# Performance work log

Hardware: AMD Instinct MI355X
Metric: run time of the kernel (lower is better)

## Reference

```python
import jax, jax.numpy as jnp
import numpy as np

EPS = 1e-5

def _ln(x, g, b):
    m = jnp.mean(x, axis=-1, keepdims=True)
    v = jnp.var(x, axis=-1, keepdims=True)
    return (x - m) / jnp.sqrt(v + EPS) * g + b

def setup_inputs() -> dict:
    key = jax.random.key(0)
    ks = jax.random.split(key, 16)
    B, N, CZ, C = 1, 512, 128, 16
    s_cz = 1.0 / np.sqrt(CZ)
    s_c = 1.0 / np.sqrt(C)
    def lin(k, fan_in, shape):
        return jax.random.uniform(k, shape, jnp.float32, -1.0, 1.0) / np.sqrt(fan_in)
    return {
        'x': jax.random.normal(ks[0], (B, N, N, CZ), jnp.float32),
        'Wa1': lin(ks[1], CZ, (CZ, C)), 'ba1': lin(ks[2], CZ, (C,)),
        'Wa2': lin(ks[3], CZ, (CZ, C)), 'ba2': lin(ks[4], CZ, (C,)),
        'Wb1': lin(ks[5], CZ, (CZ, C)), 'bb1': lin(ks[6], CZ, (C,)),
        'Wb2': lin(ks[7], CZ, (CZ, C)), 'bb2': lin(ks[8], CZ, (C,)),
        'ln2_g': jnp.ones((C,), jnp.float32), 'ln2_b': jnp.zeros((C,), jnp.float32),
        'Wg': lin(ks[9], CZ, (CZ, CZ)), 'bg': lin(ks[10], CZ, (CZ,)),
        'Wz': lin(ks[11], C, (C, CZ)), 'bz': lin(ks[12], C, (CZ,)),
    }

def reference(x, Wa1, ba1, Wa2, ba2, Wb1, bb1, Wb2, bb2, ln2_g, ln2_b, Wg, bg, Wz, bz):
    # NOTE: original code computes z=ln1(x) then overwrites z=x, so ln1 is a no-op.
    direction = 'outgoing'
    a = jax.nn.sigmoid((x @ Wa1 + ba1) * (x @ Wa2 + ba2))  # [B,N,N,c]
    b = jax.nn.sigmoid((x @ Wb1 + bb1) * (x @ Wb2 + bb2))  # [B,N,N,c]
    if direction == 'incoming':
        a = jnp.swapaxes(a, 1, 2)
        b = jnp.swapaxes(b, 1, 2)
    g = jax.nn.sigmoid(x @ Wg + bg)  # [B,N,N,c_z]
    # z[b,i,j,c] = sum_k a[b,i,k,c] * b[b,k,j,c]  (per-channel triangle matmul)
    z = jnp.einsum('bikc,bkjc->bijc', a, b)
    return g * (_ln(z, ln2_g, ln2_b) @ Wz + bz)
```

## Files before the change

### kernel.cpp

```cpp
#include <hip/hip_runtime.h>


#define NN 512
#define PP (NN*NN)
#define CZD 128
#define CD 16
#define LN_EPS 1e-5f

typedef unsigned short u16;
typedef __bf16 bf16x8 __attribute__((ext_vector_type(8)));
typedef float  f32x4  __attribute__((ext_vector_type(4)));

#define OFF_A  0u
#define OFF_B  8388608u
#define OFF_Z  16777216u
#define OFF_G  33554432u
#define OFF_WT 100663296u
#define OFF_BC 100712448u

__device__ __forceinline__ float bf2f(u16 u) {
    union { unsigned int i; float f; } v; v.i = ((unsigned int)u) << 16; return v.f;
}
__device__ __forceinline__ u16 f2bf(float f) {
    union { __bf16 b; u16 u; } v; v.b = (__bf16)f; return v.u;
}
__device__ __forceinline__ float sigmoidf(float x) { return 1.0f / (1.0f + __expf(-x)); }

__device__ __forceinline__ int swz(int row, int bytecol) {
    return row * 256 + ((((bytecol >> 4) + row) & 15) << 4) + (bytecol & 15);
}

__global__ void pack_w(const float* __restrict__ Wa1, const float* __restrict__ Wa2,
                       const float* __restrict__ Wb1, const float* __restrict__ Wb2,
                       const float* __restrict__ Wg,
                       const float* __restrict__ ba1, const float* __restrict__ ba2,
                       const float* __restrict__ bb1, const float* __restrict__ bb2,
                       const float* __restrict__ bg,
                       u16* __restrict__ wt, float* __restrict__ bc) {
    int idx = blockIdx.x * 256 + threadIdx.x;
    int n = idx >> 7, k = idx & 127;
    float v;
    if      (n < 16) v = Wa1[k * CD + n];
    else if (n < 32) v = Wa2[k * CD + (n - 16)];
    else if (n < 48) v = Wb1[k * CD + (n - 32)];
    else if (n < 64) v = Wb2[k * CD + (n - 48)];
    else             v = Wg [k * CZD + (n - 64)];
    wt[n * CZD + k] = f2bf(v);
    if (idx < 192) {
        float b;
        if      (idx < 16) b = ba1[idx];
        else if (idx < 32) b = ba2[idx - 16];
        else if (idx < 48) b = bb1[idx - 32];
        else if (idx < 64) b = bb2[idx - 48];
        else               b = bg [idx - 64];
        bc[idx] = b;
    }
}

__global__ __launch_bounds__(512, 4) void proj_kernel(const float* __restrict__ x,
                                                      const u16* __restrict__ wt,
                                                      const float* __restrict__ bc,
                                                      u16* __restrict__ a_ws, u16* __restrict__ b_ws,
                                                      u16* __restrict__ g_ws) {
    __shared__ __align__(16) char lds[49152];
    char* Wl = lds;
    char* aT = lds;
    char* bT = lds + 4096;
    char* gT = lds + 8192;
    const int t = threadIdx.x;
    const int wv = t >> 6, lane = t & 63, l16 = lane & 15, quad = lane >> 4;
    const long pos0 = (long)blockIdx.x * 128;

    const float* xrow = x + (pos0 + wv * 16 + l16) * CZD + quad * 8;
    float4 xa[4][2];
#pragma unroll
    for (int ks = 0; ks < 4; ++ks) {
        xa[ks][0] = *reinterpret_cast<const float4*>(xrow + ks * 32);
        xa[ks][1] = *reinterpret_cast<const float4*>(xrow + ks * 32 + 4);
    }

#pragma unroll
    for (int i = 0; i < 6; ++i) {
        int c = t + 512 * i;
        int n = c >> 4, g = c & 15;
        uint4 v = *reinterpret_cast<const uint4*>(wt + n * CZD + g * 8);
        *reinterpret_cast<uint4*>(Wl + swz(n, g * 16)) = v;
    }

    bf16x8 af[4];
#pragma unroll
    for (int ks = 0; ks < 4; ++ks) {
        union { u16 s[8]; bf16x8 v; } tb;
        tb.s[0] = f2bf(xa[ks][0].x); tb.s[1] = f2bf(xa[ks][0].y);
        tb.s[2] = f2bf(xa[ks][0].z); tb.s[3] = f2bf(xa[ks][0].w);
        tb.s[4] = f2bf(xa[ks][1].x); tb.s[5] = f2bf(xa[ks][1].y);
        tb.s[6] = f2bf(xa[ks][1].z); tb.s[7] = f2bf(xa[ks][1].w);
        af[ks] = tb.v;
    }
    __syncthreads();

    f32x4 acc[12];
#pragma unroll
    for (int ct = 0; ct < 12; ++ct) acc[ct] = (f32x4){0.f, 0.f, 0.f, 0.f};
#pragma unroll
    for (int ks = 0; ks < 4; ++ks)
#pragma unroll
        for (int ct = 0; ct < 12; ++ct) {
            bf16x8 wb = *reinterpret_cast<const bf16x8*>(Wl + swz(ct * 16 + l16, ks * 64 + quad * 16));
            acc[ct] = __builtin_amdgcn_mfma_f32_16x16x32_bf16(af[ks], wb, acc[ct], 0, 0, 0);
        }
    __syncthreads();

    {
        const float ba1 = bc[l16], ba2 = bc[16 + l16], bb1 = bc[32 + l16], bb2 = bc[48 + l16];
        u16 av[4], bv[4];
#pragma unroll
        for (int r = 0; r < 4; ++r) {
            av[r] = f2bf(sigmoidf((acc[0][r] + ba1) * (acc[1][r] + ba2)));
            bv[r] = f2bf(sigmoidf((acc[2][r] + bb1) * (acc[3][r] + bb2)));
        }
        *reinterpret_cast<uint2*>(aT + swz(l16, wv * 32 + quad * 8)) = *reinterpret_cast<const uint2*>(av);
        *reinterpret_cast<uint2*>(bT + swz(l16, wv * 32 + quad * 8)) = *reinterpret_cast<const uint2*>(bv);
#pragma unroll
        for (int ct = 0; ct < 8; ++ct) {
            const float bgv = bc[64 + ct * 16 + l16];
#pragma unroll
            for (int r = 0; r < 4; ++r) {
                int pos = wv * 16 + quad * 4 + r;
                *reinterpret_cast<u16*>(gT + swz(pos, ct * 32 + l16 * 2)) =
                    f2bf(sigmoidf(acc[4 + ct][r] + bgv));
            }
        }
    }
    __syncthreads();

    if (t < 256) {
        int ch = t >> 4, i = t & 15;
        uint4 v = *reinterpret_cast<const uint4*>(aT + swz(ch, i * 16));
        *reinterpret_cast<uint4*>(a_ws + (long)ch * PP + pos0 + i * 8) = v;
    } else {
        int u = t - 256;
        int ch = u >> 4, i = u & 15;
        uint4 v = *reinterpret_cast<const uint4*>(bT + swz(ch, i * 16));
        *reinterpret_cast<uint4*>(b_ws + (long)ch * PP + pos0 + i * 8) = v;
    }
#pragma unroll
    for (int i = 0; i < 4; ++i) {
        int c = t + 512 * i;
        int pos = c >> 4, g = c & 15;
        uint4 v = *reinterpret_cast<const uint4*>(gT + swz(pos, g * 16));
        *reinterpret_cast<uint4*>(g_ws + (pos0 + pos) * CZD + g * 8) = v;
    }
}

__global__ __launch_bounds__(512) void tri_kernel(const u16* __restrict__ a_ws,
                                                  const u16* __restrict__ b_ws,
                                                  float* __restrict__ z_ws) {
    __shared__ __align__(16) char Alds[16384];
    __shared__ __align__(16) char Btl [16384];
    const int t = threadIdx.x;
    const int wv = t >> 6, lane = t & 63, l16 = lane & 15, quad = lane >> 4;
    const int wr = wv >> 2, wc = wv & 3;
    const int c = blockIdx.y;
    const int i0 = (blockIdx.x >> 2) * 128, j0 = (blockIdx.x & 3) * 128;
    const u16* Ap = a_ws + (long)c * PP;
    const u16* Bp = b_ws + (long)c * PP;

    f32x4 acc[4][2];
#pragma unroll
    for (int m = 0; m < 4; ++m)
#pragma unroll
        for (int n = 0; n < 2; ++n) acc[m][n] = (f32x4){0.f, 0.f, 0.f, 0.f};

    for (int k0 = 0; k0 < NN; k0 += 64) {
#pragma unroll
        for (int i = 0; i < 2; ++i) {
            int ch = t + 512 * i;
            int r = ch >> 3, ko = (ch & 7) * 8;
            uint4 v = *reinterpret_cast<const uint4*>(Ap + (long)(i0 + r) * NN + k0 + ko);
            *reinterpret_cast<uint4*>(Alds + r * 128 + ((ko * 2) ^ ((r & 7) << 4))) = v;
        }
#pragma unroll
        for (int i = 0; i < 2; ++i) {
            int chk = t + 512 * i;
            int k = chk >> 4, jo = (chk & 15) * 8;
            union { uint4 v; u16 s[8]; } tb;
            tb.v = *reinterpret_cast<const uint4*>(Bp + (long)(k0 + k) * NN + j0 + jo);
            const int kg = k >> 3, kl = (k & 7) * 2;
#pragma unroll
            for (int jj = 0; jj < 8; ++jj) {
                int j = jo + jj;
                int gran = ((kg ^ (j & 7)) + (j >> 3)) & 7;
                *reinterpret_cast<u16*>(Btl + j * 128 + gran * 16 + kl) = tb.s[jj];
            }
        }
        __syncthreads();
#pragma unroll
        for (int ks = 0; ks < 2; ++ks) {
            bf16x8 af[4];
#pragma unroll
            for (int m = 0; m < 4; ++m) {
                int row = wr * 64 + m * 16 + l16;
                af[m] = *reinterpret_cast<const bf16x8*>(
                    Alds + row * 128 + ((ks * 64 + quad * 16) ^ ((row & 7) << 4)));
            }
#pragma unroll
            for (int n = 0; n < 2; ++n) {
                int jrow = wc * 32 + n * 16 + l16;
                int gran = (((ks * 4 + quad) ^ (jrow & 7)) + (jrow >> 3)) & 7;
                bf16x8 bf = *reinterpret_cast<const bf16x8*>(Btl + jrow * 128 + gran * 16);
#pragma unroll
                for (int m = 0; m < 4; ++m)
                    acc[m][n] = __builtin_amdgcn_mfma_f32_16x16x32_bf16(af[m], bf, acc[m][n], 0, 0, 0);
            }
        }
        __syncthreads();
    }
    float* Zp = z_ws + (long)c * PP;
#pragma unroll
    for (int m = 0; m < 4; ++m)
#pragma unroll
        for (int n = 0; n < 2; ++n)
#pragma unroll
            for (int r = 0; r < 4; ++r)
                Zp[(long)(i0 + wr * 64 + m * 16 + quad * 4 + r) * NN + j0 + wc * 32 + n * 16 + l16]
                    = acc[m][n][r];
}

__global__ __launch_bounds__(512) void out_kernel(const float* __restrict__ z_ws,
                                                  const u16* __restrict__ g_ws,
                                                  const float* __restrict__ Wz, const float* __restrict__ bz,
                                                  const float* __restrict__ lng, const float* __restrict__ lnb,
                                                  float* __restrict__ out) {
    __shared__ __align__(16) float zt[16][128];
    __shared__ __align__(16) float nl[128][20];
    __shared__ __align__(16) float wzs[16][128];
    __shared__ float bzl[128];
    __shared__ float lg[16], lb[16];
    const int t = threadIdx.x;
    const long tbase = (long)blockIdx.x * 256;

    const int zch = t >> 5, zoff = (t & 31) * 4;
    const float* zp = z_ws + (long)zch * PP + tbase + zoff;
    const float4 zv0 = *reinterpret_cast<const float4*>(zp);
    const float4 zv1 = *reinterpret_cast<const float4*>(zp + 128);

    {
        int idx = t * 4;
        const float4 v = *reinterpret_cast<const float4*>(Wz + idx);
        *reinterpret_cast<float4*>(&wzs[idx >> 7][idx & 127]) = v;
    }
    if (t < 128)      bzl[t] = bz[t];
    else if (t < 144) lg[t - 128] = lng[t - 128];
    else if (t < 160) lb[t - 144] = lnb[t - 144];
    *reinterpret_cast<float4*>(&zt[zch][zoff]) = zv0;
    __syncthreads();

    const int czp = (t & 63) * 2, pg = t >> 6;
    float wzr[32];
#pragma unroll
    for (int c0 = 0; c0 < 16; ++c0) {
        wzr[2 * c0]     = wzs[c0][czp];
        wzr[2 * c0 + 1] = wzs[c0][czp + 1];
    }
    const float bz0 = bzl[czp], bz1 = bzl[czp + 1];
    const unsigned int* gp = reinterpret_cast<const unsigned int*>(g_ws);

#pragma unroll
    for (int it = 0; it < 2; ++it) {
        const long pos0 = tbase + it * 128;
        {
            int p = t & 127, cgr = t >> 7;
            float m = 0.f;
#pragma unroll
            for (int c0 = 0; c0 < 16; ++c0) m += zt[c0][p];
            m *= (1.f / 16.f);
            float v = 0.f;
#pragma unroll
            for (int c0 = 0; c0 < 16; ++c0) { float d = zt[c0][p] - m; v += d * d; }
            v *= (1.f / 16.f);
            float s = rsqrtf(v + LN_EPS);
#pragma unroll
            for (int cc = 0; cc < 4; ++cc) {
                int c0 = cgr * 4 + cc;
                nl[p][c0] = (zt[c0][p] - m) * s * lg[c0] + lb[c0];
            }
        }
        __syncthreads();
        if (it == 0)
            *reinterpret_cast<float4*>(&zt[zch][zoff]) = zv1;

#pragma unroll
        for (int pp2 = 0; pp2 < 16; ++pp2) {
            int p = pg * 16 + pp2;
            const float4* np = reinterpret_cast<const float4*>(&nl[p][0]);
            float y0 = bz0, y1 = bz1;
#pragma unroll
            for (int c4 = 0; c4 < 4; ++c4) {
                float4 nv = np[c4];
                y0 += nv.x * wzr[(c4 * 4 + 0) * 2] + nv.y * wzr[(c4 * 4 + 1) * 2] +
                      nv.z * wzr[(c4 * 4 + 2) * 2] + nv.w * wzr[(c4 * 4 + 3) * 2];
                y1 += nv.x * wzr[(c4 * 4 + 0) * 2 + 1] + nv.y * wzr[(c4 * 4 + 1) * 2 + 1] +
                      nv.z * wzr[(c4 * 4 + 2) * 2 + 1] + nv.w * wzr[(c4 * 4 + 3) * 2 + 1];
            }
            long o = (pos0 + p) * CZD + czp;
            unsigned int gg = gp[o >> 1];
            float g0 = bf2f((u16)(gg & 0xffffu));
            float g1 = bf2f((u16)(gg >> 16));
            float2 res; res.x = g0 * y0; res.y = g1 * y1;
            *reinterpret_cast<float2*>(out + o) = res;
        }
        __syncthreads();
    }
}

extern "C" void kernel_launch(void* const* d_in, const int* in_sizes, int n_in,
                              void* d_out, int out_size, void* d_ws, size_t ws_size,
                              hipStream_t stream) {
    const float* x   = (const float*)d_in[0];
    const float* Wa1 = (const float*)d_in[1];
    const float* ba1 = (const float*)d_in[2];
    const float* Wa2 = (const float*)d_in[3];
    const float* ba2 = (const float*)d_in[4];
    const float* Wb1 = (const float*)d_in[5];
    const float* bb1 = (const float*)d_in[6];
    const float* Wb2 = (const float*)d_in[7];
    const float* bb2 = (const float*)d_in[8];
    const float* lng = (const float*)d_in[9];
    const float* lnb = (const float*)d_in[10];
    const float* Wg  = (const float*)d_in[11];
    const float* bg  = (const float*)d_in[12];
    const float* Wz  = (const float*)d_in[13];
    const float* bz  = (const float*)d_in[14];
    float* out = (float*)d_out;
    char* ws = (char*)d_ws;
    u16*   a_ws = (u16*)(ws + OFF_A);
    u16*   b_ws = (u16*)(ws + OFF_B);
    float* z_ws = (float*)(ws + OFF_Z);
    u16*   g_ws = (u16*)(ws + OFF_G);
    u16*   wt   = (u16*)(ws + OFF_WT);
    float* bc   = (float*)(ws + OFF_BC);

    hipLaunchKernelGGL(pack_w, dim3(96), dim3(256), 0, stream,
                       Wa1, Wa2, Wb1, Wb2, Wg, ba1, ba2, bb1, bb2, bg, wt, bc);
    hipLaunchKernelGGL(proj_kernel, dim3(2048), dim3(512), 0, stream, x, wt, bc, a_ws, b_ws, g_ws);
    hipLaunchKernelGGL(tri_kernel, dim3(16, 16), dim3(512), 0, stream, a_ws, b_ws, z_ws);
    hipLaunchKernelGGL(out_kernel, dim3(1024), dim3(512), 0, stream, z_ws, g_ws, Wz, bz, lng, lnb, out);
}
```

Measured before the change: 310.2 us.

## Make projection kernel persistent over 4 tiles with prefetch; pack B transpose stores

Each proj_kernel block now handles 512 positions in four sub-tiles instead of 128. The packed weights are loaded into LDS once per block and reused across all four, and x for the next sub-tile is prefetched while the current MFMAs run. Outputs are written straight to global memory instead of being staged through LDS, which drops two barriers but makes the a/b and g stores narrow and scattered. Separately, the tri_kernel B-tile transpose now loads two k rows per thread and writes packed 32-bit pairs to LDS, halving the number of scattered 16-bit stores.

Result: slower. 318.6 us (+2.7%).

```diff
diff --git a/kernel.cpp b/kernel.cpp
--- a/kernel.cpp
+++ b/kernel.cpp
@@ -62,14 +62,15 @@
                                                       const float* __restrict__ bc,
                                                       u16* __restrict__ a_ws, u16* __restrict__ b_ws,
                                                       u16* __restrict__ g_ws) {
-    __shared__ __align__(16) char lds[49152];
-    char* Wl = lds;
-    char* aT = lds;
-    char* bT = lds + 4096;
-    char* gT = lds + 8192;
+    __shared__ __align__(16) char Wl[49152];
     const int t = threadIdx.x;
     const int wv = t >> 6, lane = t & 63, l16 = lane & 15, quad = lane >> 4;
-    const long pos0 = (long)blockIdx.x * 128;
+    const long pos0 = (long)blockIdx.x * 512;
+
+    const float ba1 = bc[l16], ba2 = bc[16 + l16], bb1 = bc[32 + l16], bb2 = bc[48 + l16];
+    float bgv[8];
+#pragma unroll
+    for (int ct = 0; ct < 8; ++ct) bgv[ct] = bc[64 + ct * 16 + l16];
 
     const float* xrow = x + (pos0 + wv * 16 + l16) * CZD + quad * 8;
     float4 xa[4][2];
@@ -99,57 +100,58 @@
     }
     __syncthreads();
 
-    f32x4 acc[12];
-#pragma unroll
-    for (int ct = 0; ct < 12; ++ct) acc[ct] = (f32x4){0.f, 0.f, 0.f, 0.f};
-#pragma unroll
-    for (int ks = 0; ks < 4; ++ks)
-#pragma unroll
-        for (int ct = 0; ct < 12; ++ct) {
-            bf16x8 wb = *reinterpret_cast<const bf16x8*>(Wl + swz(ct * 16 + l16, ks * 64 + quad * 16));
-            acc[ct] = __builtin_amdgcn_mfma_f32_16x16x32_bf16(af[ks], wb, acc[ct], 0, 0, 0);
-        }
-    __syncthreads();
-
-    {
-        const float ba1 = bc[l16], ba2 = bc[16 + l16], bb1 = bc[32 + l16], bb2 = bc[48 + l16];
-        u16 av[4], bv[4];
-#pragma unroll
-        for (int r = 0; r < 4; ++r) {
-            av[r] = f2bf(sigmoidf((acc[0][r] + ba1) * (acc[1][r] + ba2)));
-            bv[r] = f2bf(sigmoidf((acc[2][r] + bb1) * (acc[3][r] + bb2)));
-        }
-        *reinterpret_cast<uint2*>(aT + swz(l16, wv * 32 + quad * 8)) = *reinterpret_cast<const uint2*>(av);
-        *reinterpret_cast<uint2*>(bT + swz(l16, wv * 32 + quad * 8)) = *reinterpret_cast<const uint2*>(bv);
-#pragma unroll
-        for (int ct = 0; ct < 8; ++ct) {
-            const float bgv = bc[64 + ct * 16 + l16];
+#pragma unroll
+    for (int p = 0; p < 4; ++p) {
+        const long prow = pos0 + p * 128 + wv * 16 + quad * 4;
+
+        f32x4 acc[12];
+#pragma unroll
+        for (int ct = 0; ct < 12; ++ct) acc[ct] = (f32x4){0.f, 0.f, 0.f, 0.f};
+#pragma unroll
+        for (int ks = 0; ks < 4; ++ks)
+#pragma unroll
+            for (int ct = 0; ct < 12; ++ct) {
+                bf16x8 wb = *reinterpret_cast<const bf16x8*>(Wl + swz(ct * 16 + l16, ks * 64 + quad * 16));
+                acc[ct] = __builtin_amdgcn_mfma_f32_16x16x32_bf16(af[ks], wb, acc[ct], 0, 0, 0);
+            }
+
+        if (p < 3) {
+            const float* xr2 = xrow + (p + 1) * 128 * CZD;
+#pragma unroll
+            for (int ks = 0; ks < 4; ++ks) {
+                xa[ks][0] = *reinterpret_cast<const float4*>(xr2 + ks * 32);
+                xa[ks][1] = *reinterpret_cast<const float4*>(xr2 + ks * 32 + 4);
+            }
+        }
+
+        {
+            u16 av[4], bv[4];
 #pragma unroll
             for (int r = 0; r < 4; ++r) {
-                int pos = wv * 16 + quad * 4 + r;
-                *reinterpret_cast<u16*>(gT + swz(pos, ct * 32 + l16 * 2)) =
-                    f2bf(sigmoidf(acc[4 + ct][r] + bgv));
-            }
-        }
-    }
-    __syncthreads();
-
-    if (t < 256) {
-        int ch = t >> 4, i = t & 15;
-        uint4 v = *reinterpret_cast<const uint4*>(aT + swz(ch, i * 16));
-        *reinterpret_cast<uint4*>(a_ws + (long)ch * PP + pos0 + i * 8) = v;
-    } else {
-        int u = t - 256;
-        int ch = u >> 4, i = u & 15;
-        uint4 v = *reinterpret_cast<const uint4*>(bT + swz(ch, i * 16));
-        *reinterpret_cast<uint4*>(b_ws + (long)ch * PP + pos0 + i * 8) = v;
-    }
-#pragma unroll
-    for (int i = 0; i < 4; ++i) {
-        int c = t + 512 * i;
-        int pos = c >> 4, g = c & 15;
-        uint4 v = *reinterpret_cast<const uint4*>(gT + swz(pos, g * 16));
-        *reinterpret_cast<uint4*>(g_ws + (pos0 + pos) * CZD + g * 8) = v;
+                av[r] = f2bf(sigmoidf((acc[0][r] + ba1) * (acc[1][r] + ba2)));
+                bv[r] = f2bf(sigmoidf((acc[2][r] + bb1) * (acc[3][r] + bb2)));
+            }
+            *reinterpret_cast<uint2*>(a_ws + (long)l16 * PP + prow) = *reinterpret_cast<const uint2*>(av);
+            *reinterpret_cast<uint2*>(b_ws + (long)l16 * PP + prow) = *reinterpret_cast<const uint2*>(bv);
+            u16* gbase = g_ws + prow * CZD + l16;
+#pragma unroll
+            for (int ct = 0; ct < 8; ++ct)
+#pragma unroll
+                for (int r = 0; r < 4; ++r)
+                    gbase[r * CZD + ct * 16] = f2bf(sigmoidf(acc[4 + ct][r] + bgv[ct]));
+        }
+
+        if (p < 3) {
+#pragma unroll
+            for (int ks = 0; ks < 4; ++ks) {
+                union { u16 s[8]; bf16x8 v; } tb;
+                tb.s[0] = f2bf(xa[ks][0].x); tb.s[1] = f2bf(xa[ks][0].y);
+                tb.s[2] = f2bf(xa[ks][0].z); tb.s[3] = f2bf(xa[ks][0].w);
+                tb.s[4] = f2bf(xa[ks][1].x); tb.s[5] = f2bf(xa[ks][1].y);
+                tb.s[6] = f2bf(xa[ks][1].z); tb.s[7] = f2bf(xa[ks][1].w);
+                af[ks] = tb.v;
+            }
+        }
     }
 }
 
@@ -180,18 +182,19 @@
             uint4 v = *reinterpret_cast<const uint4*>(Ap + (long)(i0 + r) * NN + k0 + ko);
             *reinterpret_cast<uint4*>(Alds + r * 128 + ((ko * 2) ^ ((r & 7) << 4))) = v;
         }
-#pragma unroll
-        for (int i = 0; i < 2; ++i) {
-            int chk = t + 512 * i;
-            int k = chk >> 4, jo = (chk & 15) * 8;
-            union { uint4 v; u16 s[8]; } tb;
-            tb.v = *reinterpret_cast<const uint4*>(Bp + (long)(k0 + k) * NN + j0 + jo);
+        {
+            int kp = t >> 4, jo = (t & 15) * 8;
+            int k = kp * 2;
+            union { uint4 v; u16 s[8]; } t0, t1;
+            t0.v = *reinterpret_cast<const uint4*>(Bp + (long)(k0 + k) * NN + j0 + jo);
+            t1.v = *reinterpret_cast<const uint4*>(Bp + (long)(k0 + k + 1) * NN + j0 + jo);
             const int kg = k >> 3, kl = (k & 7) * 2;
 #pragma unroll
             for (int jj = 0; jj < 8; ++jj) {
                 int j = jo + jj;
                 int gran = ((kg ^ (j & 7)) + (j >> 3)) & 7;
-                *reinterpret_cast<u16*>(Btl + j * 128 + gran * 16 + kl) = tb.s[jj];
+                unsigned int pk = (unsigned int)t0.s[jj] | ((unsigned int)t1.s[jj] << 16);
+                *reinterpret_cast<unsigned int*>(Btl + j * 128 + gran * 16 + kl) = pk;
             }
         }
         __syncthreads();
@@ -343,7 +346,7 @@
 
     hipLaunchKernelGGL(pack_w, dim3(96), dim3(256), 0, stream,
                        Wa1, Wa2, Wb1, Wb2, Wg, ba1, ba2, bb1, bb2, bg, wt, bc);
-    hipLaunchKernelGGL(proj_kernel, dim3(2048), dim3(512), 0, stream, x, wt, bc, a_ws, b_ws, g_ws);
+    hipLaunchKernelGGL(proj_kernel, dim3(512), dim3(512), 0, stream, x, wt, bc, a_ws, b_ws, g_ws);
     hipLaunchKernelGGL(tri_kernel, dim3(16, 16), dim3(512), 0, stream, a_ws, b_ws, z_ws);
     hipLaunchKernelGGL(out_kernel, dim3(1024), dim3(512), 0, stream, z_ws, g_ws, Wz, bz, lng, lnb, out);
 }
```

## Prefetch next K-tile into registers and pack B transpose stores as 32-bit

Applied to the files above, without the earlier changes.

The triangle-matmul kernel now issues the global loads for the next 64-wide K tile right after the barrier, so they overlap with the MFMA work on the current tile, instead of loading and then storing synchronously at the top of each iteration. The B tile thread mapping changes so each thread loads two adjacent k rows and writes packed 32-bit pairs into the transposed LDS layout, which halves the number of scalar LDS stores. This costs extra registers for the prefetch buffers, which may affect occupancy at 512 threads per block.

After: 308.5 us (median of 2 runs). Within noise of the previous version (-0.5%).

```diff
diff --git a/kernel.cpp b/kernel.cpp
--- a/kernel.cpp
+++ b/kernel.cpp
@@ -166,35 +166,46 @@
     const u16* Ap = a_ws + (long)c * PP;
     const u16* Bp = b_ws + (long)c * PP;
 
+    const int ar0 = t >> 3,          ako0 = (t & 7) * 8;
+    const int ar1 = (t + 512) >> 3,  ako1 = ((t + 512) & 7) * 8;
+    const int bk  = (t >> 4) * 2,    bjo  = (t & 15) * 8;
+    const int bkg = bk >> 3,         bkl  = (bk & 7) * 2;
+
     f32x4 acc[4][2];
 #pragma unroll
     for (int m = 0; m < 4; ++m)
 #pragma unroll
         for (int n = 0; n < 2; ++n) acc[m][n] = (f32x4){0.f, 0.f, 0.f, 0.f};
 
-    for (int k0 = 0; k0 < NN; k0 += 64) {
-#pragma unroll
-        for (int i = 0; i < 2; ++i) {
-            int ch = t + 512 * i;
-            int r = ch >> 3, ko = (ch & 7) * 8;
-            uint4 v = *reinterpret_cast<const uint4*>(Ap + (long)(i0 + r) * NN + k0 + ko);
-            *reinterpret_cast<uint4*>(Alds + r * 128 + ((ko * 2) ^ ((r & 7) << 4))) = v;
-        }
-#pragma unroll
-        for (int i = 0; i < 2; ++i) {
-            int chk = t + 512 * i;
-            int k = chk >> 4, jo = (chk & 15) * 8;
-            union { uint4 v; u16 s[8]; } tb;
-            tb.v = *reinterpret_cast<const uint4*>(Bp + (long)(k0 + k) * NN + j0 + jo);
-            const int kg = k >> 3, kl = (k & 7) * 2;
+    uint4 aR0 = *reinterpret_cast<const uint4*>(Ap + (long)(i0 + ar0) * NN + ako0);
+    uint4 aR1 = *reinterpret_cast<const uint4*>(Ap + (long)(i0 + ar1) * NN + ako1);
+    uint4 bR0 = *reinterpret_cast<const uint4*>(Bp + (long)(bk)     * NN + j0 + bjo);
+    uint4 bR1 = *reinterpret_cast<const uint4*>(Bp + (long)(bk + 1) * NN + j0 + bjo);
+
+    for (int s = 0; s < 8; ++s) {
+        *reinterpret_cast<uint4*>(Alds + ar0 * 128 + ((ako0 * 2) ^ ((ar0 & 7) << 4))) = aR0;
+        *reinterpret_cast<uint4*>(Alds + ar1 * 128 + ((ako1 * 2) ^ ((ar1 & 7) << 4))) = aR1;
+        {
+            union { uint4 v; u16 sh[8]; } t0, t1;
+            t0.v = bR0; t1.v = bR1;
 #pragma unroll
             for (int jj = 0; jj < 8; ++jj) {
-                int j = jo + jj;
-                int gran = ((kg ^ (j & 7)) + (j >> 3)) & 7;
-                *reinterpret_cast<u16*>(Btl + j * 128 + gran * 16 + kl) = tb.s[jj];
+                int j = bjo + jj;
+                int gran = ((bkg ^ (j & 7)) + (j >> 3)) & 7;
+                unsigned int pk = (unsigned int)t0.sh[jj] | ((unsigned int)t1.sh[jj] << 16);
+                *reinterpret_cast<unsigned int*>(Btl + j * 128 + gran * 16 + bkl) = pk;
             }
         }
         __syncthreads();
+
+        if (s < 7) {
+            const int kn = (s + 1) * 64;
+            aR0 = *reinterpret_cast<const uint4*>(Ap + (long)(i0 + ar0) * NN + kn + ako0);
+            aR1 = *reinterpret_cast<const uint4*>(Ap + (long)(i0 + ar1) * NN + kn + ako1);
+            bR0 = *reinterpret_cast<const uint4*>(Bp + (long)(kn + bk)     * NN + j0 + bjo);
+            bR1 = *reinterpret_cast<const uint4*>(Bp + (long)(kn + bk + 1) * NN + j0 + bjo);
+        }
+
 #pragma unroll
         for (int ks = 0; ks < 2; ++ks) {
             bf16x8 af[4];
```
